# Optimization experiments

Hardware: AMD Instinct MI355X
Metric: run time of the kernel (lower is better)

The kernel has to match this reference:

```python
import jax, jax.numpy as jnp
import numpy as np

L, HID, H, D = 2, 128, 8, 16  # layers, hidden, heads, head_dim
N, E = 50000, 800000
CLAMP = 5.0
BN_SCALE = 1.0 / np.sqrt(1.0 + 1e-5)  # eval BN with running mean 0, var 1


def signed_sqrt(s):
    # sqrt(relu(s)) - sqrt(relu(-s)), with safe gradients at 0
    pos = jnp.sqrt(jnp.where(s > 0, s, 1.0))
    neg = jnp.sqrt(jnp.where(s < 0, -s, 1.0))
    return jnp.where(s > 0, pos, 0.0) - jnp.where(s < 0, neg, 0.0)


def setup_inputs() -> dict:
    key = jax.random.key(0)
    ks = jax.random.split(key, 32)
    sc = 0.05
    inp = {
        "x": jax.random.normal(ks[0], (N, HID), jnp.float32),
        "edge_index": jax.random.randint(ks[1], (2, E), 0, N, jnp.int64)
        if jax.config.jax_enable_x64 else jax.random.randint(ks[1], (2, E), 0, N, jnp.int32),
        "edge_attr": jax.random.normal(ks[2], (E, HID), jnp.float32),
        "Wq": jax.random.normal(ks[3], (L, HID, HID), jnp.float32) * sc,
        "bq": jnp.zeros((L, HID), jnp.float32),
        "Wk": jax.random.normal(ks[4], (L, HID, HID), jnp.float32) * sc,
        "Wv": jax.random.normal(ks[5], (L, HID, HID), jnp.float32) * sc,
        "We": jax.random.normal(ks[6], (L, HID, 2 * HID), jnp.float32) * sc,
        "be": jnp.zeros((L, 2 * HID), jnp.float32),
        "Aw": jax.random.normal(ks[7], (L, D, H, 1), jnp.float32) * 0.2,
        "VeRow": jax.random.normal(ks[8], (L, D, H, D), jnp.float32) * sc,
        "Woh": jax.random.normal(ks[9], (L, HID, HID), jnp.float32) * sc,
        "boh": jnp.zeros((L, HID), jnp.float32),
        "Woe": jax.random.normal(ks[10], (L, HID, HID), jnp.float32) * sc,
        "boe": jnp.zeros((L, HID), jnp.float32),
        "deg_coef": jax.random.normal(ks[11], (L, 1, HID, 2), jnp.float32) * 0.2,
        "W1": jax.random.normal(ks[12], (L, HID, 2 * HID), jnp.float32) * sc,
        "b1": jnp.zeros((L, 2 * HID), jnp.float32),
        "W2": jax.random.normal(ks[13], (L, 2 * HID, HID), jnp.float32) * sc,
        "b2": jnp.zeros((L, HID), jnp.float32),
    }
    return inp


def _forward(x, edge_attr, edge_index, Wq, bq, Wk, Wv, We, be, Aw, VeRow,
             Woh, boh, Woe, boe, deg_coef, W1, b1, W2, b2):
    src, dst = edge_index[0], edge_index[1]
    n = x.shape[0]
    deg = jax.ops.segment_sum(jnp.ones_like(dst, jnp.float32), dst, num_segments=n)
    log_deg = jnp.log(deg + 1.0)[:, None]  # [N,1]

    for l in range(L):
        Qh = (x @ Wq[l] + bq[l]).reshape(n, H, D)
        Kh = (x @ Wk[l]).reshape(n, H, D)
        Vh = (x @ Wv[l]).reshape(n, H, D)
        Ep = (edge_attr @ We[l] + be[l]).reshape(-1, H, 2 * D)
        E_w, E_b = Ep[:, :, :D], Ep[:, :, D:]

        s = (Kh[src] + Qh[dst]) * E_w           # [E,H,D]
        s = signed_sqrt(s) + E_b
        e_t = jax.nn.relu(s)                     # [E,H,D]
        wE = e_t.reshape(-1, H * D)

        sc = jnp.einsum('ehd,dhc->ehc', e_t, Aw[l])   # [E,H,1]
        sc = jnp.clip(sc, -CLAMP, CLAMP)
        m = jax.ops.segment_max(sc, dst, num_segments=n)
        a = jnp.exp(sc - m[dst])
        denom = jax.ops.segment_sum(a, dst, num_segments=n)[dst] + 1e-16
        attn = a / denom                          # [E,H,1]

        wV = jax.ops.segment_sum(Vh[src] * attn, dst, num_segments=n)   # [N,H,D]
        rowV = jax.ops.segment_sum(e_t * attn, dst, num_segments=n)     # [N,H,D]
        wV = wV + jnp.einsum('nhd,dhc->nhc', rowV, VeRow[l])

        h = wV.reshape(n, H * D)
        h = h * deg_coef[l, :, :, 0] + (h * log_deg) * deg_coef[l, :, :, 1]
        h = h @ Woh[l] + boh[l]
        e = wE @ Woe[l] + boe[l]
        h = (x + h) * BN_SCALE
        e = (edge_attr + e) * BN_SCALE
        h2 = jax.nn.relu(h @ W1[l] + b1[l]) @ W2[l] + b2[l]
        h = (h + h2) * BN_SCALE
        x, edge_attr = h, e
    return x, edge_attr


def reference(x, edge_index, edge_attr, Wq, bq, Wk, Wv, We, be, Aw, VeRow,
              Woh, boh, Woe, boe, deg_coef, W1, b1, W2, b2):
    return _forward(x, edge_attr, edge_index, Wq, bq, Wk, Wv, We, be, Aw, VeRow,
                    Woh, boh, Woe, boe, deg_coef, W1, b1, W2, b2)
```

## Files before the change

### kernel.cpp

```cpp
#include <hip/hip_runtime.h>

#define NN 50000
#define NE 800000
#define CLAMPV 5.0f
#define BNS 0.9999950000374997f
#define EPKS 132
#define NBLK 49

typedef __attribute__((ext_vector_type(8))) short s16x8;
typedef __attribute__((ext_vector_type(8))) __bf16 bf16x8;
typedef __attribute__((ext_vector_type(4))) float f32x4;

__device__ inline f32x4 mfma16(s16x8 a, s16x8 b, f32x4 c) {
    return __builtin_amdgcn_mfma_f32_16x16x32_bf16(
        __builtin_bit_cast(bf16x8, a), __builtin_bit_cast(bf16x8, b), c, 0, 0, 0);
}

__device__ inline unsigned short bf16r(float f) {
    return __builtin_bit_cast(unsigned short, (__bf16)f);
}

__device__ inline int pk2(float a, float b) {
    return (int)(unsigned)bf16r(a) | ((int)(unsigned)bf16r(b) << 16);
}

__device__ inline float b2f(unsigned short u) {
    return __builtin_bit_cast(float, (unsigned)u << 16);
}


__global__ __launch_bounds__(256) void k_deg(const int* __restrict__ ei, int* __restrict__ deg) {
    int e = blockIdx.x * 256 + threadIdx.x;
    if (e < NE) atomicAdd(&deg[ei[NE + e]], 1);
}

__global__ __launch_bounds__(1024) void k_scan1(const int* __restrict__ deg, int* __restrict__ offs,
                                                int* __restrict__ bsum) {
    __shared__ int sm[1024];
    int i = blockIdx.x * 1024 + threadIdx.x;
    int v = (i < NN) ? deg[i] : 0;
    sm[threadIdx.x] = v;
    __syncthreads();
    for (int s = 1; s < 1024; s <<= 1) {
        int t = (threadIdx.x >= s) ? sm[threadIdx.x - s] : 0;
        __syncthreads();
        sm[threadIdx.x] += t;
        __syncthreads();
    }
    if (i < NN) offs[i + 1] = sm[threadIdx.x];
    if (threadIdx.x == 1023) bsum[blockIdx.x] = sm[1023];
    if (blockIdx.x == 0 && threadIdx.x == 0) offs[0] = 0;
}

__global__ void k_scan2(int* __restrict__ bsum) {
    if (threadIdx.x == 0) {
        int acc = 0;
        for (int i = 0; i < NBLK; ++i) { int v = bsum[i]; bsum[i] = acc; acc += v; }
    }
}

__global__ __launch_bounds__(1024) void k_scan3(int* __restrict__ offs, const int* __restrict__ bsum) {
    int i = blockIdx.x * 1024 + threadIdx.x;
    if (i < NN) offs[i + 1] += bsum[blockIdx.x];
}

__global__ __launch_bounds__(256) void k_fill(const int* __restrict__ ei, const int* __restrict__ offs,
                                              int* __restrict__ cursor, int* __restrict__ csr_src,
                                              int* __restrict__ epos) {
    int e = blockIdx.x * 256 + threadIdx.x;
    if (e < NE) {
        int d = ei[NE + e];
        int pos = offs[d] + atomicAdd(&cursor[d], 1);
        csr_src[pos] = ei[e];
        epos[e] = pos;
    }
}

__global__ __launch_bounds__(256) void k_logdeg(const int* __restrict__ deg, float* __restrict__ logdeg) {
    int i = blockIdx.x * 256 + threadIdx.x;
    if (i < NN) logdeg[i] = logf((float)deg[i] + 1.0f);
}

#define PL_A (128*256)
#define PL_B (128*128)
__global__ __launch_bounds__(256) void k_packAll(
    const float* __restrict__ We,  const float* __restrict__ Woe, const float* __restrict__ Wq,
    const float* __restrict__ Wk,  const float* __restrict__ Wv,  const float* __restrict__ Woh,
    const float* __restrict__ W1,  const float* __restrict__ W2,  const float* __restrict__ VR,
    short* __restrict__ Wep,  short* __restrict__ Woep, short* __restrict__ Wqp,
    short* __restrict__ Wkp,  short* __restrict__ Wvp,  short* __restrict__ Wohp,
    short* __restrict__ W1p,  short* __restrict__ W2p,  short* __restrict__ VRp) {
    int s = blockIdx.x * 256 + threadIdx.x;
    const float* W; short* out; int ncol, perL; bool vr = false;
    if (s < 2 * PL_A) { W = We; out = Wep; ncol = 256; perL = PL_A; }
    else if ((s -= 2 * PL_A) < 2 * PL_B) { W = Woe; out = Woep; ncol = 128; perL = PL_B; }
    else if ((s -= 2 * PL_B) < 2 * PL_B) { W = Wq;  out = Wqp;  ncol = 128; perL = PL_B; }
    else if ((s -= 2 * PL_B) < 2 * PL_B) { W = Wk;  out = Wkp;  ncol = 128; perL = PL_B; }
    else if ((s -= 2 * PL_B) < 2 * PL_B) { W = Wv;  out = Wvp;  ncol = 128; perL = PL_B; }
    else if ((s -= 2 * PL_B) < 2 * PL_B) { W = Woh; out = Wohp; ncol = 128; perL = PL_B; }
    else if ((s -= 2 * PL_B) < 2 * PL_A) { W = W1;  out = W1p;  ncol = 256; perL = PL_A; }
    else if ((s -= 2 * PL_A) < 2 * PL_A) { W = W2;  out = W2p;  ncol = 128; perL = PL_A; }
    else if ((s -= 2 * PL_A) < 2 * PL_B) { W = VR;  out = VRp;  ncol = 128; perL = PL_B; vr = true; }
    else return;
    int l = s / perL, q = s % perL;
    int j = q & 7; int t2 = q >> 3; int kg = t2 & 3; t2 >>= 2;
    int col = t2 % ncol; int kt = t2 / ncol;
    int k = kt * 32 + kg * 8 + j;
    float v;
    if (vr) v = ((k >> 4) == (col >> 4)) ? VR[l * 2048 + (k & 15) * 128 + col] : 0.f;
    else    v = W[(size_t)l * perL + k * ncol + col];
    out[(size_t)l * perL + q] = (short)bf16r(v);
}


__global__ __launch_bounds__(512) void k_qkv(const float* __restrict__ x,
                                             const short* __restrict__ Wqp, const float* __restrict__ bq,
                                             const short* __restrict__ Wkp, const short* __restrict__ Wvp,
                                             unsigned short* __restrict__ Qh, unsigned short* __restrict__ Kh,
                                             unsigned short* __restrict__ Vh) {
    __shared__ short xsw[64 * 128];
    int t = threadIdx.x;
    int ci = t & 15, r0 = t >> 4;
    int n0 = blockIdx.x * 64;
    for (int rr = r0; rr < 64; rr += 32) {
        int n = n0 + rr;
        int4 pkv = make_int4(0, 0, 0, 0);
        if (n < NN) {
            const float4* src = (const float4*)(x + (size_t)n * 128 + ci * 8);
            float4 v0 = src[0], v1 = src[1];
            pkv.x = pk2(v0.x, v0.y); pkv.y = pk2(v0.z, v0.w);
            pkv.z = pk2(v1.x, v1.y); pkv.w = pk2(v1.z, v1.w);
        }
        int byte = (rr * 256 + ci * 16) ^ ((rr & 7) << 4);
        *(int4*)((char*)xsw + byte) = pkv;
    }
    __syncthreads();
    int lane = t & 63, w = t >> 6;
    int l15 = lane & 15, kg = lane >> 4;
    f32x4 acc[4][3];
#pragma unroll
    for (int m = 0; m < 4; ++m)
#pragma unroll
        for (int q = 0; q < 3; ++q) { acc[m][q][0] = 0.f; acc[m][q][1] = 0.f; acc[m][q][2] = 0.f; acc[m][q][3] = 0.f; }
    int col = w * 16 + l15;
#pragma unroll
    for (int kt = 0; kt < 4; ++kt) {
        s16x8 a[4];
#pragma unroll
        for (int m = 0; m < 4; ++m) {
            int row = m * 16 + l15;
            int abyte = (row * 256 + kt * 64 + kg * 16) ^ ((l15 & 7) << 4);
            a[m] = *(const s16x8*)((const char*)xsw + abyte);
        }
        size_t bo = ((size_t)((kt * 128 + col) * 4 + kg)) * 8;
        s16x8 bqf = *(const s16x8*)(Wqp + bo);
        s16x8 bkf = *(const s16x8*)(Wkp + bo);
        s16x8 bvf = *(const s16x8*)(Wvp + bo);
#pragma unroll
        for (int m = 0; m < 4; ++m) {
            acc[m][0] = mfma16(a[m], bqf, acc[m][0]);
            acc[m][1] = mfma16(a[m], bkf, acc[m][1]);
            acc[m][2] = mfma16(a[m], bvf, acc[m][2]);
        }
    }
    float bqv = bq[col];
#pragma unroll
    for (int m = 0; m < 4; ++m)
#pragma unroll
        for (int i = 0; i < 4; ++i) {
            int n = n0 + m * 16 + kg * 4 + i;
            if (n < NN) {
                Qh[(size_t)n * 128 + col] = bf16r(acc[m][0][i] + bqv);
                Kh[(size_t)n * 128 + col] = bf16r(acc[m][1][i]);
                Vh[(size_t)n * 128 + col] = bf16r(acc[m][2][i]);
            }
        }
}

template<bool IN_F32>
__global__ __launch_bounds__(512) void k_edgeA(const void* __restrict__ ea_, const int* __restrict__ ei,
                                               const int* __restrict__ epos,
                                               const short* __restrict__ Wep, const float* __restrict__ be,
                                               const float* __restrict__ Aw,
                                               const unsigned short* __restrict__ Qh,
                                               const unsigned short* __restrict__ Kh,
                                               unsigned short* __restrict__ e_t, float* __restrict__ sc,
                                               const short* __restrict__ Woep, const float* __restrict__ boe,
                                               void* __restrict__ eout_) {
    __shared__ short eas[64 * 128];
    __shared__ int epts[64 * EPKS];
    const float* eaf = (const float*)ea_;
    const unsigned short* eab = (const unsigned short*)ea_;
    unsigned short* eout_b = (unsigned short*)eout_;
    float* eout_f = (float*)eout_;

    int e0 = blockIdx.x * 64;
    int t = threadIdx.x;
    int ci = t & 15, r0 = t >> 4;
    int eA = e0 + r0, eB = eA + 32;
    int siA = ei[eA], diA = ei[NE + eA], posA = epos[eA];
    int siB = ei[eB], diB = ei[NE + eB], posB = epos[eB];

    {
#pragma unroll
        for (int h = 0; h < 2; ++h) {
            int rr = r0 + h * 32;
            int4 pkv;
            if (IN_F32) {
                const float4* src = (const float4*)(eaf + (size_t)(e0 + rr) * 128 + ci * 8);
                float4 v0 = src[0], v1 = src[1];
                pkv.x = pk2(v0.x, v0.y); pkv.y = pk2(v0.z, v0.w);
                pkv.z = pk2(v1.x, v1.y); pkv.w = pk2(v1.z, v1.w);
            } else {
                pkv = *(const int4*)(eab + (size_t)(e0 + rr) * 128 + ci * 8);
            }
            int byte = (rr * 256 + ci * 16) ^ ((rr & 7) << 4);
            *(int4*)((char*)eas + byte) = pkv;
        }
    }
    __syncthreads();
    union { int4 v; unsigned short us[8]; } kuA, quA, kuB, quB;
    kuA.v = *(const int4*)(Kh + (size_t)siA * 128 + ci * 8);
    quA.v = *(const int4*)(Qh + (size_t)diA * 128 + ci * 8);
    kuB.v = *(const int4*)(Kh + (size_t)siB * 128 + ci * 8);
    quB.v = *(const int4*)(Qh + (size_t)diB * 128 + ci * 8);

    int lane = t & 63, w = t >> 6;
    int l15 = lane & 15, kg = lane >> 4;
    {
        f32x4 acc[4][2];
#pragma unroll
        for (int m = 0; m < 4; ++m)
#pragma unroll
            for (int q = 0; q < 2; ++q) { acc[m][q][0] = 0.f; acc[m][q][1] = 0.f; acc[m][q][2] = 0.f; acc[m][q][3] = 0.f; }
#pragma unroll
        for (int kt = 0; kt < 4; ++kt) {
            s16x8 a[4];
#pragma unroll
            for (int m = 0; m < 4; ++m) {
                int row = m * 16 + l15;
                int abyte = (row * 256 + kt * 64 + kg * 16) ^ ((l15 & 7) << 4);
                a[m] = *(const s16x8*)((const char*)eas + abyte);
            }
#pragma unroll
            for (int q = 0; q < 2; ++q) {
                int col = w * 32 + q * 16 + l15;
                s16x8 b = *(const s16x8*)(Wep + ((size_t)((kt * 256 + col) * 4 + kg)) * 8);
#pragma unroll
                for (int m = 0; m < 4; ++m) acc[m][q] = mfma16(a[m], b, acc[m][q]);
            }
        }
        float bw = be[w * 32 + l15], bb = be[w * 32 + 16 + l15];
#pragma unroll
        for (int m = 0; m < 4; ++m)
#pragma unroll
            for (int i = 0; i < 4; ++i) {
                int row = m * 16 + kg * 4 + i;
                epts[row * EPKS + w * 16 + l15] = pk2(acc[m][0][i] + bw, acc[m][1][i] + bb);
            }
    }
    __syncthreads();
    int4 wA0, wA1, wB0, wB1;
    {
        const int4* pA = (const int4*)(epts + r0 * EPKS + ci * 8);
        wA0 = pA[0]; wA1 = pA[1];
        const int4* pB = (const int4*)(epts + (r0 + 32) * EPKS + ci * 8);
        wB0 = pB[0]; wB1 = pB[1];
    }
    __syncthreads();
    {
        int hh = ci >> 1, dbase = (ci & 1) * 8;
        float aw[8];
#pragma unroll
        for (int j = 0; j < 8; ++j) aw[j] = Aw[(dbase + j) * 8 + hh];
#pragma unroll
        for (int h = 0; h < 2; ++h) {
            int r = r0 + h * 32;
            int pos = h ? posB : posA;
            const unsigned short* kus = h ? kuB.us : kuA.us;
            const unsigned short* qus = h ? quB.us : quA.us;
            const int4 w0 = h ? wB0 : wA0;
            const int4 w1 = h ? wB1 : wA1;
            int prs[8] = {w0.x, w0.y, w0.z, w0.w, w1.x, w1.y, w1.z, w1.w};
            float p = 0.f;
            float etv[8];
#pragma unroll
            for (int j = 0; j < 8; ++j) {
                int pr = prs[j];
                float ew = b2f((unsigned short)pr);
                float ebv = b2f((unsigned short)((unsigned)pr >> 16));
                float kq = b2f(kus[j]) + b2f(qus[j]);
                float sv = kq * ew;
                float ss = copysignf(sqrtf(fabsf(sv)), sv);
                float et = fmaxf(ss + ebv, 0.f);
                etv[j] = et;
                p += et * aw[j];
            }
            int4 pkv;
            pkv.x = pk2(etv[0], etv[1]); pkv.y = pk2(etv[2], etv[3]);
            pkv.z = pk2(etv[4], etv[5]); pkv.w = pk2(etv[6], etv[7]);
            *(int4*)(e_t + (size_t)pos * 128 + ci * 8) = pkv;
            int byte = (r * 256 + ci * 16) ^ ((r & 7) << 4);
            *(int4*)((char*)epts + byte) = pkv;
            p += __shfl_xor(p, 1);
            if ((ci & 1) == 0) {
                float s = fminf(fmaxf(p, -CLAMPV), CLAMPV);
                sc[(size_t)pos * 8 + hh] = s;
            }
        }
    }
    __syncthreads();
    {
        f32x4 acc[4];
#pragma unroll
        for (int m = 0; m < 4; ++m) { acc[m][0] = 0.f; acc[m][1] = 0.f; acc[m][2] = 0.f; acc[m][3] = 0.f; }
        int col = w * 16 + l15;
#pragma unroll
        for (int kt = 0; kt < 4; ++kt) {
            s16x8 a[4];
#pragma unroll
            for (int m = 0; m < 4; ++m) {
                int row = m * 16 + l15;
                int abyte = (row * 256 + kt * 64 + kg * 16) ^ ((l15 & 7) << 4);
                a[m] = *(const s16x8*)((const char*)epts + abyte);
            }
            s16x8 b = *(const s16x8*)(Woep + ((size_t)((kt * 128 + col) * 4 + kg)) * 8);
#pragma unroll
            for (int m = 0; m < 4; ++m) acc[m] = mfma16(a[m], b, acc[m]);
        }
        float bb = boe[col];
#pragma unroll
        for (int m = 0; m < 4; ++m)
#pragma unroll
            for (int i = 0; i < 4; ++i) {
                int rr = m * 16 + kg * 4 + i;
                int rbyte = (rr * 256 + col * 2) ^ ((rr & 7) << 4);
                float res = b2f(*(const unsigned short*)((const char*)eas + rbyte));
                size_t idx = (size_t)(e0 + rr) * 128 + col;
                float v = (res + acc[m][i] + bb) * BNS;
                if (IN_F32) eout_b[idx] = bf16r(v);
                else        eout_f[idx] = v;
            }
    }
}

__global__ __launch_bounds__(64) void k_nattn(const int* __restrict__ offs, const int* __restrict__ csr_src,
                                              const float* __restrict__ sc,
                                              const unsigned short* __restrict__ e_t,
                                              const unsigned short* __restrict__ Vh,
                                              float* __restrict__ wV, float* __restrict__ rowV) {
    int n = blockIdx.x;
    int lane = threadIdx.x;
    int beg = offs[n], end = offs[n + 1];
    int h = lane & 7, es = lane >> 3;
    float m = -1e30f;
    for (int i = beg + es; i < end; i += 8)
        m = fmaxf(m, sc[(size_t)i * 8 + h]);
#pragma unroll
    for (int off = 8; off < 64; off <<= 1) m = fmaxf(m, __shfl_xor(m, off));
    float dsum = 0.0f;
    for (int i = beg + es; i < end; i += 8)
        dsum += expf(sc[(size_t)i * 8 + h] - m);
#pragma unroll
    for (int off = 8; off < 64; off <<= 1) dsum += __shfl_xor(dsum, off);
    float inv_d = 1.0f / (dsum + 1e-16f);

    int hv = lane >> 3;
    float mv = __shfl(m, hv);
    float idv = __shfl(inv_d, hv);
    float av0 = 0.0f, av1 = 0.0f, ar0 = 0.0f, ar1 = 0.0f;
    for (int i = beg; i < end; ++i) {
        float a = expf(sc[(size_t)i * 8 + hv] - mv) * idv;
        int s = csr_src[i];
        int v = ((const int*)Vh)[(size_t)s * 64 + lane];
        int u = ((const int*)e_t)[(size_t)i * 64 + lane];
        av0 += b2f((unsigned short)v) * a;
        av1 += b2f((unsigned short)((unsigned)v >> 16)) * a;
        ar0 += b2f((unsigned short)u) * a;
        ar1 += b2f((unsigned short)((unsigned)u >> 16)) * a;
    }
    *(float2*)(wV + (size_t)n * 128 + 2 * lane)   = make_float2(av0, av1);
    *(float2*)(rowV + (size_t)n * 128 + 2 * lane) = make_float2(ar0, ar1);
}

__global__ __launch_bounds__(512) void k_nodeB(const float* __restrict__ wV, const float* __restrict__ rowV,
                                               const short* __restrict__ VRp, const float* __restrict__ dc,
                                               const float* __restrict__ logdeg, const float* __restrict__ x,
                                               const short* __restrict__ Wohp, const float* __restrict__ boh,
                                               const short* __restrict__ W1p, const float* __restrict__ b1,
                                               const short* __restrict__ W2p, const float* __restrict__ b2,
                                               float* __restrict__ xout) {
    __shared__ short bufA[64 * 128];
    __shared__ short bufU[64 * 256];
    int n0 = blockIdx.x * 64;
    int t = threadIdx.x;
    int ci = t & 15, r0 = t >> 4;
    {
#pragma unroll
        for (int h = 0; h < 2; ++h) {
            int rr = r0 + h * 32, n = n0 + rr;
            int4 pkv = make_int4(0, 0, 0, 0);
            if (n < NN) {
                const float4* src = (const float4*)(rowV + (size_t)n * 128 + ci * 8);
                float4 v0 = src[0], v1 = src[1];
                pkv.x = pk2(v0.x, v0.y); pkv.y = pk2(v0.z, v0.w);
                pkv.z = pk2(v1.x, v1.y); pkv.w = pk2(v1.z, v1.w);
            }
            int byte = (rr * 256 + ci * 16) ^ ((rr & 7) << 4);
            *(int4*)((char*)bufA + byte) = pkv;
        }
    }
    __syncthreads();
    int lane = t & 63, w = t >> 6;
    int l15 = lane & 15, kg = lane >> 4;
    int col = w * 16 + l15;
    {
        f32x4 acc[4];
#pragma unroll
        for (int m = 0; m < 4; ++m)
#pragma unroll
            for (int i = 0; i < 4; ++i) {
                int n = n0 + m * 16 + kg * 4 + i;
                acc[m][i] = (n < NN) ? wV[(size_t)n * 128 + col] : 0.f;
            }
#pragma unroll
        for (int kt = 0; kt < 4; ++kt) {
            s16x8 a[4];
#pragma unroll
            for (int m = 0; m < 4; ++m) {
                int row = m * 16 + l15;
                int abyte = (row * 256 + kt * 64 + kg * 16) ^ ((l15 & 7) << 4);
                a[m] = *(const s16x8*)((const char*)bufA + abyte);
            }
            s16x8 b = *(const s16x8*)(VRp + ((size_t)((kt * 128 + col) * 4 + kg)) * 8);
#pragma unroll
            for (int m = 0; m < 4; ++m) acc[m] = mfma16(a[m], b, acc[m]);
        }
        float d0 = dc[col * 2], d1 = dc[col * 2 + 1];
#pragma unroll
        for (int m = 0; m < 4; ++m)
#pragma unroll
            for (int i = 0; i < 4; ++i) {
                int rr = m * 16 + kg * 4 + i, n = n0 + rr;
                float ld = (n < NN) ? logdeg[n] : 0.f;
                float hs = acc[m][i] * (d0 + ld * d1);
                int byte = (rr * 256 + col * 2) ^ ((rr & 7) << 4);
                *(unsigned short*)((char*)bufU + byte) = bf16r(hs);
            }
    }
    __syncthreads();
    float h1r[4][4];
    {
        f32x4 acc[4];
#pragma unroll
        for (int m = 0; m < 4; ++m) { acc[m][0] = 0.f; acc[m][1] = 0.f; acc[m][2] = 0.f; acc[m][3] = 0.f; }
#pragma unroll
        for (int kt = 0; kt < 4; ++kt) {
            s16x8 a[4];
#pragma unroll
            for (int m = 0; m < 4; ++m) {
                int row = m * 16 + l15;
                int abyte = (row * 256 + kt * 64 + kg * 16) ^ ((l15 & 7) << 4);
                a[m] = *(const s16x8*)((const char*)bufU + abyte);
            }
            s16x8 b = *(const s16x8*)(Wohp + ((size_t)((kt * 128 + col) * 4 + kg)) * 8);
#pragma unroll
            for (int m = 0; m < 4; ++m) acc[m] = mfma16(a[m], b, acc[m]);
        }
        float bb = boh[col];
#pragma unroll
        for (int m = 0; m < 4; ++m)
#pragma unroll
            for (int i = 0; i < 4; ++i) {
                int rr = m * 16 + kg * 4 + i, n = n0 + rr;
                float xv = (n < NN) ? x[(size_t)n * 128 + col] : 0.f;
                float h1 = (xv + acc[m][i] + bb) * BNS;
                h1r[m][i] = h1;
                int byte = (rr * 256 + col * 2) ^ ((rr & 7) << 4);
                *(unsigned short*)((char*)bufA + byte) = bf16r(h1);
            }
    }
    __syncthreads();
    {
        f32x4 acc[4][2];
#pragma unroll
        for (int m = 0; m < 4; ++m)
#pragma unroll
            for (int q = 0; q < 2; ++q) { acc[m][q][0] = 0.f; acc[m][q][1] = 0.f; acc[m][q][2] = 0.f; acc[m][q][3] = 0.f; }
#pragma unroll
        for (int kt = 0; kt < 4; ++kt) {
            s16x8 a[4];
#pragma unroll
            for (int m = 0; m < 4; ++m) {
                int row = m * 16 + l15;
                int abyte = (row * 256 + kt * 64 + kg * 16) ^ ((l15 & 7) << 4);
                a[m] = *(const s16x8*)((const char*)bufA + abyte);
            }
#pragma unroll
            for (int q = 0; q < 2; ++q) {
                int colq = w * 32 + q * 16 + l15;
                s16x8 b = *(const s16x8*)(W1p + ((size_t)((kt * 256 + colq) * 4 + kg)) * 8);
#pragma unroll
                for (int m = 0; m < 4; ++m) acc[m][q] = mfma16(a[m], b, acc[m][q]);
            }
        }
        __syncthreads();
#pragma unroll
        for (int q = 0; q < 2; ++q) {
            int colq = w * 32 + q * 16 + l15;
            float bb = b1[colq];
#pragma unroll
            for (int m = 0; m < 4; ++m)
#pragma unroll
                for (int i = 0; i < 4; ++i) {
                    int rr = m * 16 + kg * 4 + i;
                    float us = fmaxf(acc[m][q][i] + bb, 0.f);
                    int byte = (rr * 512 + colq * 2) ^ ((rr & 7) << 4);
                    *(unsigned short*)((char*)bufU + byte) = bf16r(us);
                }
        }
    }
    __syncthreads();
    {
        f32x4 acc[4];
#pragma unroll
        for (int m = 0; m < 4; ++m) { acc[m][0] = 0.f; acc[m][1] = 0.f; acc[m][2] = 0.f; acc[m][3] = 0.f; }
#pragma unroll
        for (int kt = 0; kt < 8; ++kt) {
            s16x8 a[4];
#pragma unroll
            for (int m = 0; m < 4; ++m) {
                int row = m * 16 + l15;
                int abyte = (row * 512 + kt * 64 + kg * 16) ^ ((l15 & 7) << 4);
                a[m] = *(const s16x8*)((const char*)bufU + abyte);
            }
            s16x8 b = *(const s16x8*)(W2p + ((size_t)((kt * 128 + col) * 4 + kg)) * 8);
#pragma unroll
            for (int m = 0; m < 4; ++m) acc[m] = mfma16(a[m], b, acc[m]);
        }
        float bb = b2[col];
#pragma unroll
        for (int m = 0; m < 4; ++m)
#pragma unroll
            for (int i = 0; i < 4; ++i) {
                int n = n0 + m * 16 + kg * 4 + i;
                if (n < NN) xout[(size_t)n * 128 + col] = (h1r[m][i] + acc[m][i] + bb) * BNS;
            }
    }
}


extern "C" void kernel_launch(void* const* d_in, const int* in_sizes, int n_in,
                              void* d_out, int out_size, void* d_ws, size_t ws_size,
                              hipStream_t stream) {
    (void)in_sizes; (void)n_in; (void)out_size; (void)ws_size;
    const float* x_in0  = (const float*)d_in[0];
    const int*   ei     = (const int*)d_in[1];
    const float* ea_in0 = (const float*)d_in[2];
    const float* Wq = (const float*)d_in[3];
    const float* bq = (const float*)d_in[4];
    const float* Wk = (const float*)d_in[5];
    const float* Wv = (const float*)d_in[6];
    const float* We = (const float*)d_in[7];
    const float* be = (const float*)d_in[8];
    const float* Aw = (const float*)d_in[9];
    const float* VeRow = (const float*)d_in[10];
    const float* Woh = (const float*)d_in[11];
    const float* boh = (const float*)d_in[12];
    const float* Woe = (const float*)d_in[13];
    const float* boe = (const float*)d_in[14];
    const float* dc  = (const float*)d_in[15];
    const float* W1 = (const float*)d_in[16];
    const float* b1 = (const float*)d_in[17];
    const float* W2 = (const float*)d_in[18];
    const float* b2 = (const float*)d_in[19];

    char* ws = (char*)d_ws;
    size_t off = 0;
    auto alloc = [&](size_t bytes) { void* p = ws + off; off = (off + bytes + 255) & ~(size_t)255; return p; };
    int*   deg    = (int*)alloc((size_t)NN * 4);
    int*   cursor = (int*)alloc((size_t)NN * 4);
    int*   offs   = (int*)alloc((size_t)(NN + 1) * 4);
    int*   bsum   = (int*)alloc((size_t)64 * 4);
    int*   csr_src= (int*)alloc((size_t)NE * 4);
    int*   epos   = (int*)alloc((size_t)NE * 4);
    float* logdeg = (float*)alloc((size_t)NN * 4);
    unsigned short* Qh = (unsigned short*)alloc((size_t)NN * 128 * 2);
    unsigned short* Kh = (unsigned short*)alloc((size_t)NN * 128 * 2);
    unsigned short* Vh = (unsigned short*)alloc((size_t)NN * 128 * 2);
    unsigned short* e_t = (unsigned short*)alloc((size_t)NE * 128 * 2);
    unsigned short* ea_bf = (unsigned short*)alloc((size_t)NE * 128 * 2);
    float* sc     = (float*)alloc((size_t)NE * 8 * 4);
    float* wV     = (float*)alloc((size_t)NN * 128 * 4);
    float* rowV   = (float*)alloc((size_t)NN * 128 * 4);
    short* Wep    = (short*)alloc((size_t)2 * 128 * 256 * 2);
    short* Woep   = (short*)alloc((size_t)2 * 128 * 128 * 2);
    short* Wqp    = (short*)alloc((size_t)2 * 128 * 128 * 2);
    short* Wkp    = (short*)alloc((size_t)2 * 128 * 128 * 2);
    short* Wvp    = (short*)alloc((size_t)2 * 128 * 128 * 2);
    short* Wohp   = (short*)alloc((size_t)2 * 128 * 128 * 2);
    short* W1p    = (short*)alloc((size_t)2 * 128 * 256 * 2);
    short* W2p    = (short*)alloc((size_t)2 * 256 * 128 * 2);
    short* VRp    = (short*)alloc((size_t)2 * 128 * 128 * 2);

    float* out_x = (float*)d_out;
    float* out_e = out_x + (size_t)NN * 128;

    hipError_t err;
    err = hipMemsetAsync(deg, 0, (size_t)NN * 4, stream); (void)err;
    err = hipMemsetAsync(cursor, 0, (size_t)NN * 4, stream); (void)err;

    k_deg<<<(NE + 255) / 256, 256, 0, stream>>>(ei, deg);
    k_scan1<<<NBLK, 1024, 0, stream>>>(deg, offs, bsum);
    k_scan2<<<1, 64, 0, stream>>>(bsum);
    k_scan3<<<NBLK, 1024, 0, stream>>>(offs, bsum);
    k_fill<<<(NE + 255) / 256, 256, 0, stream>>>(ei, offs, cursor, csr_src, epos);
    k_logdeg<<<(NN + 255) / 256, 256, 0, stream>>>(deg, logdeg);
    k_packAll<<<1536, 256, 0, stream>>>(We, Woe, Wq, Wk, Wv, Woh, W1, W2, VeRow,
                                        Wep, Woep, Wqp, Wkp, Wvp, Wohp, W1p, W2p, VRp);

    for (int l = 0; l < 2; ++l) {
        const float* x_l  = (l == 0) ? x_in0 : out_x;
        const short* Wqp_l = Wqp + (size_t)l * 128 * 128;
        const float* bq_l = bq + (size_t)l * 128;
        const short* Wkp_l = Wkp + (size_t)l * 128 * 128;
        const short* Wvp_l = Wvp + (size_t)l * 128 * 128;
        const short* Wep_l = Wep + (size_t)l * 128 * 256;
        const float* be_l = be + (size_t)l * 256;
        const float* Aw_l = Aw + (size_t)l * 16 * 8;
        const short* VRp_l = VRp + (size_t)l * 128 * 128;
        const short* Wohp_l = Wohp + (size_t)l * 128 * 128;
        const float* boh_l = boh + (size_t)l * 128;
        const short* Woep_l = Woep + (size_t)l * 128 * 128;
        const float* boe_l = boe + (size_t)l * 128;
        const float* dc_l  = dc + (size_t)l * 128 * 2;
        const short* W1p_l = W1p + (size_t)l * 128 * 256;
        const float* b1_l = b1 + (size_t)l * 256;
        const short* W2p_l = W2p + (size_t)l * 256 * 128;
        const float* b2_l = b2 + (size_t)l * 128;

        k_qkv<<<(NN + 63) / 64, 512, 0, stream>>>(x_l, Wqp_l, bq_l, Wkp_l, Wvp_l, Qh, Kh, Vh);
        if (l == 0) {
            k_edgeA<true><<<NE / 64, 512, 0, stream>>>(ea_in0, ei, epos, Wep_l, be_l, Aw_l, Qh, Kh,
                                                       e_t, sc, Woep_l, boe_l, ea_bf);
        } else {
            k_edgeA<false><<<NE / 64, 512, 0, stream>>>(ea_bf, ei, epos, Wep_l, be_l, Aw_l, Qh, Kh,
                                                        e_t, sc, Woep_l, boe_l, out_e);
        }
        k_nattn<<<NN, 64, 0, stream>>>(offs, csr_src, sc, e_t, Vh, wV, rowV);
        k_nodeB<<<(NN + 63) / 64, 512, 0, stream>>>(wV, rowV, VRp_l, dc_l, logdeg, x_l,
                                                    Wohp_l, boh_l, W1p_l, b1_l, W2p_l, b2_l, out_x);
    }
}
```

Measured before the change: 1.046 ms.

## Fuse node attention aggregation and next-layer QKV projection into node kernel

Merges the per-node softmax aggregation (k_nattn) into k_nodeB so wV and rowV stay in LDS instead of round-tripping through global fp32 buffers. In layer 0 the node kernel also computes the layer-1 Q/K/V projection from the freshly produced node features, removing the second k_qkv launch. The log-degree computation is folded into the scan kernel. In exchange, each 512-thread block now runs the irregular gather for 64 nodes, 8 per wave in sequence, which lowers the parallelism of that phase compared with one block per node and may cause load imbalance. Layer 1 in-place reads and writes out_x inside the same block.

```diff
diff --git a/kernel.cpp b/kernel.cpp
--- a/kernel.cpp
+++ b/kernel.cpp
@@ -35,10 +35,11 @@
 }
 
 __global__ __launch_bounds__(1024) void k_scan1(const int* __restrict__ deg, int* __restrict__ offs,
-                                                int* __restrict__ bsum) {
+                                                int* __restrict__ bsum, float* __restrict__ logdeg) {
     __shared__ int sm[1024];
     int i = blockIdx.x * 1024 + threadIdx.x;
     int v = (i < NN) ? deg[i] : 0;
+    if (i < NN) logdeg[i] = logf((float)v + 1.0f);
     sm[threadIdx.x] = v;
     __syncthreads();
     for (int s = 1; s < 1024; s <<= 1) {
@@ -74,11 +75,6 @@
         csr_src[pos] = ei[e];
         epos[e] = pos;
     }
-}
-
-__global__ __launch_bounds__(256) void k_logdeg(const int* __restrict__ deg, float* __restrict__ logdeg) {
-    int i = blockIdx.x * 256 + threadIdx.x;
-    if (i < NN) logdeg[i] = logf((float)deg[i] + 1.0f);
 }
 
 #define PL_A (128*256)
@@ -344,74 +340,63 @@
     }
 }
 
-__global__ __launch_bounds__(64) void k_nattn(const int* __restrict__ offs, const int* __restrict__ csr_src,
-                                              const float* __restrict__ sc,
-                                              const unsigned short* __restrict__ e_t,
-                                              const unsigned short* __restrict__ Vh,
-                                              float* __restrict__ wV, float* __restrict__ rowV) {
-    int n = blockIdx.x;
-    int lane = threadIdx.x;
-    int beg = offs[n], end = offs[n + 1];
-    int h = lane & 7, es = lane >> 3;
-    float m = -1e30f;
-    for (int i = beg + es; i < end; i += 8)
-        m = fmaxf(m, sc[(size_t)i * 8 + h]);
-#pragma unroll
-    for (int off = 8; off < 64; off <<= 1) m = fmaxf(m, __shfl_xor(m, off));
-    float dsum = 0.0f;
-    for (int i = beg + es; i < end; i += 8)
-        dsum += expf(sc[(size_t)i * 8 + h] - m);
-#pragma unroll
-    for (int off = 8; off < 64; off <<= 1) dsum += __shfl_xor(dsum, off);
-    float inv_d = 1.0f / (dsum + 1e-16f);
-
-    int hv = lane >> 3;
-    float mv = __shfl(m, hv);
-    float idv = __shfl(inv_d, hv);
-    float av0 = 0.0f, av1 = 0.0f, ar0 = 0.0f, ar1 = 0.0f;
-    for (int i = beg; i < end; ++i) {
-        float a = expf(sc[(size_t)i * 8 + hv] - mv) * idv;
-        int s = csr_src[i];
-        int v = ((const int*)Vh)[(size_t)s * 64 + lane];
-        int u = ((const int*)e_t)[(size_t)i * 64 + lane];
-        av0 += b2f((unsigned short)v) * a;
-        av1 += b2f((unsigned short)((unsigned)v >> 16)) * a;
-        ar0 += b2f((unsigned short)u) * a;
-        ar1 += b2f((unsigned short)((unsigned)u >> 16)) * a;
-    }
-    *(float2*)(wV + (size_t)n * 128 + 2 * lane)   = make_float2(av0, av1);
-    *(float2*)(rowV + (size_t)n * 128 + 2 * lane) = make_float2(ar0, ar1);
-}
-
-__global__ __launch_bounds__(512) void k_nodeB(const float* __restrict__ wV, const float* __restrict__ rowV,
-                                               const short* __restrict__ VRp, const float* __restrict__ dc,
-                                               const float* __restrict__ logdeg, const float* __restrict__ x,
-                                               const short* __restrict__ Wohp, const float* __restrict__ boh,
-                                               const short* __restrict__ W1p, const float* __restrict__ b1,
-                                               const short* __restrict__ W2p, const float* __restrict__ b2,
-                                               float* __restrict__ xout) {
+template<bool EMIT>
+__global__ __launch_bounds__(512) void k_nodeB(
+    const int* __restrict__ offs, const int* __restrict__ csr_src, const float* __restrict__ sc,
+    const unsigned short* __restrict__ e_t, const unsigned short* __restrict__ Vh,
+    const short* __restrict__ VRp, const float* __restrict__ dc,
+    const float* __restrict__ logdeg, const float* __restrict__ x,
+    const short* __restrict__ Wohp, const float* __restrict__ boh,
+    const short* __restrict__ W1p, const float* __restrict__ b1,
+    const short* __restrict__ W2p, const float* __restrict__ b2,
+    float* __restrict__ xout,
+    const short* __restrict__ Wqp2, const float* __restrict__ bq2,
+    const short* __restrict__ Wkp2, const short* __restrict__ Wvp2,
+    unsigned short* __restrict__ Qh2, unsigned short* __restrict__ Kh2,
+    unsigned short* __restrict__ Vh2) {
     __shared__ short bufA[64 * 128];
     __shared__ short bufU[64 * 256];
     int n0 = blockIdx.x * 64;
     int t = threadIdx.x;
-    int ci = t & 15, r0 = t >> 4;
-    {
-#pragma unroll
-        for (int h = 0; h < 2; ++h) {
-            int rr = r0 + h * 32, n = n0 + rr;
-            int4 pkv = make_int4(0, 0, 0, 0);
+    int lane = t & 63, w = t >> 6;
+    {
+        for (int j = 0; j < 8; ++j) {
+            int n = n0 + w * 8 + j;
+            float av0 = 0.f, av1 = 0.f, ar0 = 0.f, ar1 = 0.f;
             if (n < NN) {
-                const float4* src = (const float4*)(rowV + (size_t)n * 128 + ci * 8);
-                float4 v0 = src[0], v1 = src[1];
-                pkv.x = pk2(v0.x, v0.y); pkv.y = pk2(v0.z, v0.w);
-                pkv.z = pk2(v1.x, v1.y); pkv.w = pk2(v1.z, v1.w);
-            }
-            int byte = (rr * 256 + ci * 16) ^ ((rr & 7) << 4);
-            *(int4*)((char*)bufA + byte) = pkv;
-        }
-    }
-    __syncthreads();
-    int lane = t & 63, w = t >> 6;
+                int beg = offs[n], end = offs[n + 1];
+                int h = lane & 7, es = lane >> 3;
+                float mx = -1e30f;
+                for (int i = beg + es; i < end; i += 8)
+                    mx = fmaxf(mx, sc[(size_t)i * 8 + h]);
+#pragma unroll
+                for (int o = 8; o < 64; o <<= 1) mx = fmaxf(mx, __shfl_xor(mx, o));
+                float ds = 0.f;
+                for (int i = beg + es; i < end; i += 8)
+                    ds += expf(sc[(size_t)i * 8 + h] - mx);
+#pragma unroll
+                for (int o = 8; o < 64; o <<= 1) ds += __shfl_xor(ds, o);
+                float inv = 1.f / (ds + 1e-16f);
+                int hv = lane >> 3;
+                float mv = __shfl(mx, hv), idv = __shfl(inv, hv);
+                for (int i = beg; i < end; ++i) {
+                    float a = expf(sc[(size_t)i * 8 + hv] - mv) * idv;
+                    int s = csr_src[i];
+                    int v = ((const int*)Vh)[(size_t)s * 64 + lane];
+                    int u = ((const int*)e_t)[(size_t)i * 64 + lane];
+                    av0 += b2f((unsigned short)v) * a;
+                    av1 += b2f((unsigned short)((unsigned)v >> 16)) * a;
+                    ar0 += b2f((unsigned short)u) * a;
+                    ar1 += b2f((unsigned short)((unsigned)u >> 16)) * a;
+                }
+            }
+            int rr = w * 8 + j;
+            *(float2*)((char*)bufU + rr * 512 + lane * 8) = make_float2(av0, av1);
+            int byte = (rr * 256 + lane * 4) ^ ((rr & 7) << 4);
+            *(int*)((char*)bufA + byte) = pk2(ar0, ar1);
+        }
+    }
+    __syncthreads();
     int l15 = lane & 15, kg = lane >> 4;
     int col = w * 16 + l15;
     {
@@ -420,8 +405,8 @@
         for (int m = 0; m < 4; ++m)
 #pragma unroll
             for (int i = 0; i < 4; ++i) {
-                int n = n0 + m * 16 + kg * 4 + i;
-                acc[m][i] = (n < NN) ? wV[(size_t)n * 128 + col] : 0.f;
+                int rr = m * 16 + kg * 4 + i;
+                acc[m][i] = *(const float*)((const char*)bufU + rr * 512 + col * 4);
             }
 #pragma unroll
         for (int kt = 0; kt < 4; ++kt) {
@@ -436,6 +421,7 @@
 #pragma unroll
             for (int m = 0; m < 4; ++m) acc[m] = mfma16(a[m], b, acc[m]);
         }
+        __syncthreads();
         float d0 = dc[col * 2], d1 = dc[col * 2 + 1];
 #pragma unroll
         for (int m = 0; m < 4; ++m)
@@ -543,8 +529,53 @@
         for (int m = 0; m < 4; ++m)
 #pragma unroll
             for (int i = 0; i < 4; ++i) {
+                int rr = m * 16 + kg * 4 + i, n = n0 + rr;
+                float outv = (h1r[m][i] + acc[m][i] + bb) * BNS;
+                if (n < NN) xout[(size_t)n * 128 + col] = outv;
+                if (EMIT) {
+                    int byte = (rr * 256 + col * 2) ^ ((rr & 7) << 4);
+                    *(unsigned short*)((char*)bufA + byte) = bf16r(outv);
+                }
+            }
+    }
+    if (EMIT) {
+        __syncthreads();
+        f32x4 acc[4][3];
+#pragma unroll
+        for (int m = 0; m < 4; ++m)
+#pragma unroll
+            for (int q = 0; q < 3; ++q) { acc[m][q][0] = 0.f; acc[m][q][1] = 0.f; acc[m][q][2] = 0.f; acc[m][q][3] = 0.f; }
+#pragma unroll
+        for (int kt = 0; kt < 4; ++kt) {
+            s16x8 a[4];
+#pragma unroll
+            for (int m = 0; m < 4; ++m) {
+                int row = m * 16 + l15;
+                int abyte = (row * 256 + kt * 64 + kg * 16) ^ ((l15 & 7) << 4);
+                a[m] = *(const s16x8*)((const char*)bufA + abyte);
+            }
+            size_t bo = ((size_t)((kt * 128 + col) * 4 + kg)) * 8;
+            s16x8 bqf = *(const s16x8*)(Wqp2 + bo);
+            s16x8 bkf = *(const s16x8*)(Wkp2 + bo);
+            s16x8 bvf = *(const s16x8*)(Wvp2 + bo);
+#pragma unroll
+            for (int m = 0; m < 4; ++m) {
+                acc[m][0] = mfma16(a[m], bqf, acc[m][0]);
+                acc[m][1] = mfma16(a[m], bkf, acc[m][1]);
+                acc[m][2] = mfma16(a[m], bvf, acc[m][2]);
+            }
+        }
+        float bqv = bq2[col];
+#pragma unroll
+        for (int m = 0; m < 4; ++m)
+#pragma unroll
+            for (int i = 0; i < 4; ++i) {
                 int n = n0 + m * 16 + kg * 4 + i;
-                if (n < NN) xout[(size_t)n * 128 + col] = (h1r[m][i] + acc[m][i] + bb) * BNS;
+                if (n < NN) {
+                    Qh2[(size_t)n * 128 + col] = bf16r(acc[m][0][i] + bqv);
+                    Kh2[(size_t)n * 128 + col] = bf16r(acc[m][1][i]);
+                    Vh2[(size_t)n * 128 + col] = bf16r(acc[m][2][i]);
+                }
             }
     }
 }
@@ -585,14 +616,15 @@
     int*   csr_src= (int*)alloc((size_t)NE * 4);
     int*   epos   = (int*)alloc((size_t)NE * 4);
     float* logdeg = (float*)alloc((size_t)NN * 4);
-    unsigned short* Qh = (unsigned short*)alloc((size_t)NN * 128 * 2);
-    unsigned short* Kh = (unsigned short*)alloc((size_t)NN * 128 * 2);
-    unsigned short* Vh = (unsigned short*)alloc((size_t)NN * 128 * 2);
+    unsigned short* Qh  = (unsigned short*)alloc((size_t)NN * 128 * 2);
+    unsigned short* Kh  = (unsigned short*)alloc((size_t)NN * 128 * 2);
+    unsigned short* Vh  = (unsigned short*)alloc((size_t)NN * 128 * 2);
+    unsigned short* Qh2 = (unsigned short*)alloc((size_t)NN * 128 * 2);
+    unsigned short* Kh2 = (unsigned short*)alloc((size_t)NN * 128 * 2);
+    unsigned short* Vh2 = (unsigned short*)alloc((size_t)NN * 128 * 2);
     unsigned short* e_t = (unsigned short*)alloc((size_t)NE * 128 * 2);
     unsigned short* ea_bf = (unsigned short*)alloc((size_t)NE * 128 * 2);
     float* sc     = (float*)alloc((size_t)NE * 8 * 4);
-    float* wV     = (float*)alloc((size_t)NN * 128 * 4);
-    float* rowV   = (float*)alloc((size_t)NN * 128 * 4);
     short* Wep    = (short*)alloc((size_t)2 * 128 * 256 * 2);
     short* Woep   = (short*)alloc((size_t)2 * 128 * 128 * 2);
     short* Wqp    = (short*)alloc((size_t)2 * 128 * 128 * 2);
@@ -611,44 +643,26 @@
     err = hipMemsetAsync(cursor, 0, (size_t)NN * 4, stream); (void)err;
 
     k_deg<<<(NE + 255) / 256, 256, 0, stream>>>(ei, deg);
-    k_scan1<<<NBLK, 1024, 0, stream>>>(deg, offs, bsum);
+    k_scan1<<<NBLK, 1024, 0, stream>>>(deg, offs, bsum, logdeg);
     k_scan2<<<1, 64, 0, stream>>>(bsum);
     k_scan3<<<NBLK, 1024, 0, stream>>>(offs, bsum);
     k_fill<<<(NE + 255) / 256, 256, 0, stream>>>(ei, offs, cursor, csr_src, epos);
-    k_logdeg<<<(NN + 255) / 256, 256, 0, stream>>>(deg, logdeg);
     k_packAll<<<1536, 256, 0, stream>>>(We, Woe, Wq, Wk, Wv, Woh, W1, W2, VeRow,
                                         Wep, Woep, Wqp, Wkp, Wvp, Wohp, W1p, W2p, VRp);
 
-    for (int l = 0; l < 2; ++l) {
-        const float* x_l  = (l == 0) ? x_in0 : out_x;
-        const short* Wqp_l = Wqp + (size_t)l * 128 * 128;
-        const float* bq_l = bq + (size_t)l * 128;
-        const short* Wkp_l = Wkp + (size_t)l * 128 * 128;
-        const short* Wvp_l = Wvp + (size_t)l * 128 * 128;
-        const short* Wep_l = Wep + (size_t)l * 128 * 256;
-        const float* be_l = be + (size_t)l * 256;
-        const float* Aw_l = Aw + (size_t)l * 16 * 8;
-        const short* VRp_l = VRp + (size_t)l * 128 * 128;
-        const short* Wohp_l = Wohp + (size_t)l * 128 * 128;
-        const float* boh_l = boh + (size_t)l * 128;
-        const short* Woep_l = Woep + (size_t)l * 128 * 128;
-        const float* boe_l = boe + (size_t)l * 128;
-        const float* dc_l  = dc + (size_t)l * 128 * 2;
-        const short* W1p_l = W1p + (size_t)l * 128 * 256;
-        const float* b1_l = b1 + (size_t)l * 256;
-        const short* W2p_l = W2p + (size_t)l * 256 * 128;
-        const float* b2_l = b2 + (size_t)l * 128;
-
-        k_qkv<<<(NN + 63) / 64, 512, 0, stream>>>(x_l, Wqp_l, bq_l, Wkp_l, Wvp_l, Qh, Kh, Vh);
-        if (l == 0) {
-            k_edgeA<true><<<NE / 64, 512, 0, stream>>>(ea_in0, ei, epos, Wep_l, be_l, Aw_l, Qh, Kh,
-                                                       e_t, sc, Woep_l, boe_l, ea_bf);
-        } else {
-            k_edgeA<false><<<NE / 64, 512, 0, stream>>>(ea_bf, ei, epos, Wep_l, be_l, Aw_l, Qh, Kh,
-                                                        e_t, sc, Woep_l, boe_l, out_e);
-        }
-        k_nattn<<<NN, 64, 0, stream>>>(offs, csr_src, sc, e_t, Vh, wV, rowV);
-        k_nodeB<<<(NN + 63) / 64, 512, 0, stream>>>(wV, rowV, VRp_l, dc_l, logdeg, x_l,
-                                                    Wohp_l, boh_l, W1p_l, b1_l, W2p_l, b2_l, out_x);
-    }
-}
+    k_qkv<<<(NN + 63) / 64, 512, 0, stream>>>(x_in0, Wqp, bq, Wkp, Wvp, Qh, Kh, Vh);
+    k_edgeA<true><<<NE / 64, 512, 0, stream>>>(ea_in0, ei, epos, Wep, be, Aw, Qh, Kh,
+                                               e_t, sc, Woep, boe, ea_bf);
+    k_nodeB<true><<<(NN + 63) / 64, 512, 0, stream>>>(
+        offs, csr_src, sc, e_t, Vh, VRp, dc, logdeg, x_in0,
+        Wohp, boh, W1p, b1, W2p, b2, out_x,
+        Wqp + 128 * 128, bq + 128, Wkp + 128 * 128, Wvp + 128 * 128, Qh2, Kh2, Vh2);
+
+    k_edgeA<false><<<NE / 64, 512, 0, stream>>>(ea_bf, ei, epos, Wep + 128 * 256, be + 256,
+                                                Aw + 128, Qh2, Kh2, e_t, sc,
+                                                Woep + 128 * 128, boe + 128, out_e);
+    k_nodeB<false><<<(NN + 63) / 64, 512, 0, stream>>>(
+        offs, csr_src, sc, e_t, Vh2, VRp + 128 * 128, dc + 256, logdeg, out_x,
+        Wohp + 128 * 128, boh + 128, W1p + 128 * 256, b1 + 256, W2p + 256 * 128, b2 + 128, out_x,
+        nullptr, nullptr, nullptr, nullptr, nullptr, nullptr, nullptr);
+}
```

Result: slower. 1.663 ms (+58.9%).
